# Performance work log

Measured on AMD Instinct MI355X. Metric: run time of the kernel, lower is better.

The kernel has to match this reference:

```python
import jax, jax.numpy as jnp
import numpy as np

NUM_HEADS = 12
WINDOW = 128
LOOK_B = 1
LOOK_F = 1


def look_around(x, pad_value):
    # x: (b, n_windows, window, ...) ; pad along window axis (axis=1), concat along axis=2
    pads = [(0, 0), (LOOK_B, LOOK_F)] + [(0, 0)] * (x.ndim - 2)
    p = jnp.pad(x, pads, constant_values=pad_value)
    n = x.shape[1]
    return jnp.concatenate([p[:, i:i + n] for i in range(LOOK_B + LOOK_F + 1)], axis=2)


def split_heads(x):
    # (L, B, D) -> (B*H, L, hd), batch-major over heads (index = b*H + h)
    L, B, D = x.shape
    return jnp.transpose(x.reshape(L, B * NUM_HEADS, D // NUM_HEADS), (1, 0, 2))


def merge_heads(x):
    # (B*H, L, hd) -> (L, B, D)
    BH, L, hd = x.shape
    return jnp.transpose(x, (1, 0, 2)).reshape(L, BH // NUM_HEADS, hd * NUM_HEADS)


def setup_inputs() -> dict:
    key = jax.random.key(0)
    ks = jax.random.split(key, 12)
    S, B, D = 4096, 8, 768
    inp = {
        'hidden_states': jax.random.normal(ks[0], (S, B, D), dtype=jnp.float32),
        'key_padding_mask': jax.random.bernoulli(ks[1], 0.2, (B, S)),
    }
    scale = 0.02
    for i, name in enumerate(['Wq', 'Wk', 'Wv', 'Wgq']):
        inp[name] = jax.random.normal(ks[2 + i], (D, D), dtype=jnp.float32) * scale
    for i, name in enumerate(['bq', 'bk', 'bv', 'bgq']):
        inp[name] = jax.random.normal(ks[6 + i], (D,), dtype=jnp.float32) * scale
    return inp


def reference(hidden_states, key_padding_mask, Wq, bq, Wk, bk, Wv, bv, Wgq, bgq):
    S, B, D = hidden_states.shape
    H, W = NUM_HEADS, WINDOW
    hd = D // H
    n = S // W
    BH = B * H
    neg = -jnp.finfo(hidden_states.dtype).max
    inv_sqrt = hd ** (-0.5)

    q = split_heads(hidden_states @ Wq + bq)  # (BH, S, hd)
    k = split_heads(hidden_states @ Wk + bk)
    v = split_heads(hidden_states @ Wv + bv)

    # --- local windowed attention ---
    bq_ = q.reshape(BH, n, W, hd)
    bk_ = look_around(k.reshape(BH, n, W, hd), 0.0)   # (BH, n, 3W, hd)
    bv_ = look_around(v.reshape(BH, n, W, hd), 0.0)
    dots = jnp.einsum('bnie,bnje->bnij', bq_, bk_) * inv_sqrt  # (BH, n, W, 3W)

    im = key_padding_mask.reshape(B, n, W)
    km = look_around(im, True)                        # (B, n, 3W), pads masked
    mask = im[:, :, :, None] | km[:, :, None, :]      # (B, n, W, 3W)
    mask = jnp.broadcast_to(mask[:, None], (B, H, n, W, 3 * W)).reshape(BH, n, W, 3 * W)
    dots = jnp.where(mask, neg, dots)
    attn = jax.nn.softmax(dots, axis=-1)
    out = jnp.einsum('bnij,bnje->bnie', attn, bv_).reshape(BH, S, hd)
    out = merge_heads(out)                            # (S, B, D)

    # --- global-token attention (token 0 attends to everything) ---
    gq = split_heads(hidden_states[0:1] @ Wgq + bgq)  # (BH, 1, hd)
    gdots = jnp.einsum('bie,bje->bij', gq, k) * inv_sqrt  # (BH, 1, S)
    gmask = jnp.broadcast_to(key_padding_mask[:, None], (B, H, S)).reshape(BH, S)
    gdots = jnp.where(gmask[:, None, :], neg, gdots)
    gattn = jax.nn.softmax(gdots, axis=-1)
    gout = merge_heads(jnp.einsum('bij,bje->bie', gattn, v))  # (1, B, D)

    return out.at[0].set(gout[0])
```

## Files before the change

kernel.cpp:

```cpp
#include <hip/hip_runtime.h>
#include <float.h>

#define S_  4096
#define B_  8
#define D_  768
#define H_  12
#define HD_ 64
#define W_  128
#define BH_ 96
#define SB_ 32768

typedef unsigned short u16;
typedef __attribute__((ext_vector_type(8))) short bf16x8;
typedef __attribute__((ext_vector_type(4))) float f32x4;

#define MFMA16(a,b,c) __builtin_amdgcn_mfma_f32_16x16x32_bf16(a,b,c,0,0,0)

__device__ __forceinline__ u16 f2bf(float x){
  unsigned int u = __float_as_uint(x);
  return (u16)((u + 0x7FFFu + ((u >> 16) & 1u)) >> 16);
}
__device__ __forceinline__ float bf2f(unsigned int lo16){ return __uint_as_float(lo16 << 16); }
__device__ __forceinline__ float bflo(unsigned int u){ return __uint_as_float(u << 16); }
__device__ __forceinline__ float bfhi(unsigned int u){ return __uint_as_float(u & 0xFFFF0000u); }
__device__ __forceinline__ unsigned int pk2(float a, float b){
  return (unsigned int)f2bf(a) | ((unsigned int)f2bf(b) << 16);
}

__device__ __forceinline__ void gload_lds16(const void* g, void* l){
  __builtin_amdgcn_global_load_lds(
      (const __attribute__((address_space(1))) void*)g,
      (__attribute__((address_space(3))) void*)l, 16, 0, 0);
}

__device__ __forceinline__ bool mask_at(const void* mp, int flag, int idx){
  return flag ? (((const unsigned char*)mp)[idx] != 0)
              : (((const unsigned int*)mp)[idx] != 0u);
}

__global__ __launch_bounds__(256) void prep_kernel(
    const float* __restrict__ hid, const float* __restrict__ W0,
    const float* __restrict__ W1, const float* __restrict__ W2,
    const unsigned int* __restrict__ maskw,
    u16* __restrict__ hb, u16* __restrict__ wT, int* __restrict__ flag){
  __shared__ float tile[64][65];
  const int bid = blockIdx.x, t = threadIdx.x;
  if (bid < 2048){
    int idx = bid * 256 + t;
    for (int base = idx * 8; base < 25165824; base += 2048 * 256 * 8){
      float4 a = *(const float4*)&hid[base];
      float4 b = *(const float4*)&hid[base + 4];
      uint4 o;
      o.x = pk2(a.x, a.y); o.y = pk2(a.z, a.w);
      o.z = pk2(b.x, b.y); o.w = pk2(b.z, b.w);
      *(uint4*)&hb[base] = o;
    }
  } else if (bid < 2480){
    const int wb = bid - 2048;
    const int mat = wb / 144, r2 = wb % 144;
    const int kt0 = (r2 / 12) * 64, nt0 = (r2 % 12) * 64;
    const float* Wsel = mat == 0 ? W0 : (mat == 1 ? W1 : W2);
    { const int row = t >> 2, c16 = (t & 3) * 16;
#pragma unroll
      for (int j = 0; j < 4; ++j){
        float4 v = *(const float4*)&Wsel[(size_t)(kt0 + row) * 768 + nt0 + c16 + j * 4];
        tile[row][c16 + j*4 + 0] = v.x; tile[row][c16 + j*4 + 1] = v.y;
        tile[row][c16 + j*4 + 2] = v.z; tile[row][c16 + j*4 + 3] = v.w;
      } }
    __syncthreads();
    { const int nl = t >> 2, k16 = (t & 3) * 16;
      unsigned int o[8];
#pragma unroll
      for (int j = 0; j < 8; ++j)
        o[j] = pk2(tile[k16 + 2*j][nl], tile[k16 + 2*j + 1][nl]);
      u16* dst = wT + (size_t)mat * 589824 + (size_t)(nt0 + nl) * 768 + kt0 + k16;
      *(uint4*)dst       = make_uint4(o[0], o[1], o[2], o[3]);
      *(uint4*)(dst + 8) = make_uint4(o[4], o[5], o[6], o[7]); }
  } else {
    unsigned int* red = (unsigned int*)&tile[0][0];
    unsigned int acc = 0u;
    for (int i = t; i < 8192; i += 256) acc |= maskw[i];
    red[t] = acc;
    __syncthreads();
    for (int s = 128; s > 0; s >>= 1){
      if (t < s) red[t] |= red[t + s];
      __syncthreads();
    }
    if (t == 0){
      unsigned int o = red[0];
      *flag = (o > 1u && (o & 0xFEFEFEFEu) == 0u) ? 1 : 0;
    }
  }
}

__global__ __launch_bounds__(256) void proj_mfma_kernel(
    const u16* __restrict__ hb, const u16* __restrict__ wT,
    const float* __restrict__ bq, const float* __restrict__ bk, const float* __restrict__ bv,
    u16* __restrict__ qb, u16* __restrict__ kb, u16* __restrict__ vb,
    u16* __restrict__ vtb){
  __shared__ union ShMem {
    struct { u16 A0[8192]; u16 B0[8192]; u16 A1[8192]; u16 B1[8192]; } ab;
    u16 C[128 * 130];
  } sh;
  const int t = threadIdx.x;
  const int id = blockIdx.x;
  const int xcd = id & 7, loc = id >> 3;
  const int nt = loc % 18;
  const int mt = xcd * 32 + loc / 18;
  const int p  = nt / 6;
  const int c0 = (nt % 6) * 128;
  const int r0 = mt * 128;
  const float* bias = p == 0 ? bq : (p == 1 ? bk : bv);
  u16* dst = p == 0 ? qb : (p == 1 ? kb : vb);
  const u16* wTp = wT + (size_t)p * 589824;

  const int lane = t & 63, w = t >> 6;
  const int l15 = lane & 15, lg = lane >> 4;
  const int wr = w >> 1, wc = w & 1;
  const int lrc = lane >> 3, slot = lane & 7;

  f32x4 acc[4][4] = {};

#define PSTAGE(AS, BS, kof) do{ \
    _Pragma("unroll") \
    for (int c = 0; c < 4; ++c){ \
      int chunk = w * 4 + c; \
      int ldsrow = chunk * 8 + lrc; \
      int slotg = slot ^ (ldsrow & 7); \
      gload_lds16(&hb [(size_t)(r0 + ldsrow) * 768 + (kof) + slotg * 8], &AS[chunk * 512]); \
      gload_lds16(&wTp[(size_t)(c0 + ldsrow) * 768 + (kof) + slotg * 8], &BS[chunk * 512]); \
    } \
  }while(0)

#define PITER(AS, BS, kof, VNSTR, DOSTAGE) do{ \
    asm volatile("s_waitcnt vmcnt(" VNSTR ")" ::: "memory"); \
    __builtin_amdgcn_sched_barrier(0); \
    __builtin_amdgcn_s_barrier(); \
    bf16x8 af[4][2], bf[4][2]; \
    _Pragma("unroll") \
    for (int mf = 0; mf < 4; ++mf) \
      _Pragma("unroll") \
      for (int ks = 0; ks < 2; ++ks) \
        af[mf][ks] = *(const bf16x8*)&AS[(wr*64 + mf*16 + l15) * 64 + (((ks*4 + lg) ^ (l15 & 7)) * 8)]; \
    _Pragma("unroll") \
    for (int nf = 0; nf < 4; ++nf) \
      _Pragma("unroll") \
      for (int ks = 0; ks < 2; ++ks) \
        bf[nf][ks] = *(const bf16x8*)&BS[(wc*64 + nf*16 + l15) * 64 + (((ks*4 + lg) ^ (l15 & 7)) * 8)]; \
    asm volatile("s_waitcnt lgkmcnt(0)" ::: "memory"); \
    __builtin_amdgcn_sched_barrier(0); \
    __builtin_amdgcn_s_barrier(); \
    if (DOSTAGE) PSTAGE(AS, BS, (kof) + 128); \
    _Pragma("unroll") \
    for (int ks = 0; ks < 2; ++ks) \
      _Pragma("unroll") \
      for (int mf = 0; mf < 4; ++mf) \
        _Pragma("unroll") \
        for (int nf = 0; nf < 4; ++nf) \
          acc[mf][nf] = MFMA16(af[mf][ks], bf[nf][ks], acc[mf][nf]); \
  }while(0)

  PSTAGE(sh.ab.A0, sh.ab.B0, 0);
  PSTAGE(sh.ab.A1, sh.ab.B1, 64);
  for (int i2 = 0; i2 < 5; ++i2){
    const int kc = i2 * 128;
    PITER(sh.ab.A0, sh.ab.B0, kc,      "8", 1);
    PITER(sh.ab.A1, sh.ab.B1, kc + 64, "8", 1);
  }
  PITER(sh.ab.A0, sh.ab.B0, 640, "8", 0);
  PITER(sh.ab.A1, sh.ab.B1, 704, "0", 0);
#undef PSTAGE
#undef PITER

#pragma unroll
  for (int nf = 0; nf < 4; ++nf){
    int c = c0 + wc*64 + nf*16 + l15;
    float bsv = bias[c];
#pragma unroll
    for (int mf = 0; mf < 4; ++mf)
#pragma unroll
      for (int r = 0; r < 4; ++r)
        sh.C[(wr*64 + mf*16 + lg*4 + r) * 130 + wc*64 + nf*16 + l15] = f2bf(acc[mf][nf][r] + bsv);
  }
  __syncthreads();
  { const int b = t >> 5, hh2 = (t >> 4) & 1, sl = t & 15;
    const int srow0 = r0 >> 3;
    const int hh = (c0 >> 6) + hh2;
    u16* dp = dst + ((size_t)(b * 12 + hh) * 4096 + srow0 + sl) * 64;
    const u16* sp = &sh.C[(sl * 8 + b) * 130 + hh2 * 64];
#pragma unroll
    for (int j = 0; j < 8; ++j)
      *(uint4*)(dp + j*8) = *(const uint4*)(sp + j*8);
  }
  if (p == 2){
    const int ri0 = t * 4;
#pragma unroll
    for (int j = 0; j < 4; ++j){
      const int ri = ri0 + j;
      const int b = ri >> 7, hh2 = (ri >> 6) & 1, dd = ri & 63;
      unsigned int o[8];
#pragma unroll
      for (int q = 0; q < 8; ++q){
        unsigned int lo = sh.C[((2*q    )*8 + b) * 130 + hh2*64 + dd];
        unsigned int hi = sh.C[((2*q + 1)*8 + b) * 130 + hh2*64 + dd];
        o[q] = lo | (hi << 16);
      }
      u16* dp2 = vtb + ((size_t)((b*12 + (c0 >> 6) + hh2) * 64) + dd) * 4096 + (r0 >> 3);
      *(uint4*)dp2       = make_uint4(o[0], o[1], o[2], o[3]);
      *(uint4*)(dp2 + 8) = make_uint4(o[4], o[5], o[6], o[7]);
    }
  }
}

__global__ __launch_bounds__(256) void local_mfma_kernel(
    const u16* __restrict__ qb, const u16* __restrict__ kb, const u16* __restrict__ vtb,
    const void* __restrict__ maskp, const int* __restrict__ flagp,
    float* __restrict__ out){
  __shared__ u16 KsA[64 * 64], KsB[64 * 64];
  __shared__ u16 VsA[64 * 64], VsB[64 * 64];
  __shared__ u16 Ps[4][32][72];
  __shared__ float kpen[384];
  __shared__ float qpen_s[128];
  const int t = threadIdx.x;
  const int id = blockIdx.x;
  const int swz = (id & 7) * 384 + (id >> 3);
  const int n_i = swz & 31, bh = swz >> 5;
  const int b_i = bh / 12, h = bh % 12;
  const int flag = *flagp;
  const int w = t >> 6, lane = t & 63, l15 = lane & 15, lg = lane >> 4;
  const int lrc = lane >> 3, slot = lane & 7;
  const int jbase0 = n_i * 128 - 128;
  const int jt_lo = (n_i == 0) ? 2 : 0;
  const int jt_hi = (n_i == 31) ? 4 : 6;

#define STAGE_TILE(KS, VS, jtv) do{ \
    int jb_ = jbase0 + (jtv) * 64; \
    _Pragma("unroll") \
    for (int c = 0; c < 2; ++c){ \
      int chunk = w * 2 + c; \
      int ldsrow = chunk * 8 + lrc; \
      int slotg = slot ^ (ldsrow & 7); \
      gload_lds16(&kb [((size_t)bh * 4096 + jb_ + ldsrow) * 64 + slotg * 8], &KS[chunk * 512]); \
      gload_lds16(&vtb[((size_t)bh * 64 + ldsrow) * 4096 + jb_ + slotg * 8], &VS[chunk * 512]); \
    } \
  }while(0)

#define COMPUTE_TILE(KS, VS, jtv) do{ \
    f32x4 dt[2][4] = {}; \
    __builtin_amdgcn_s_setprio(1); \
    _Pragma("unroll") \
    for (int ks2 = 0; ks2 < 2; ++ks2) \
      _Pragma("unroll") \
      for (int nf = 0; nf < 4; ++nf){ \
        bf16x8 bk_ = *(const bf16x8*)&KS[(nf*16 + l15) * 64 + (((ks2*4 + lg) ^ (l15 & 7)) * 8)]; \
        dt[0][nf] = MFMA16(bk_, aq[0][ks2], dt[0][nf]);    \
        dt[1][nf] = MFMA16(bk_, aq[1][ks2], dt[1][nf]); \
      } \
    __builtin_amdgcn_s_setprio(0); \
     \
    _Pragma("unroll") \
    for (int nf = 0; nf < 4; ++nf){ \
      float4 kpv = *(const float4*)&kpen[(jtv)*64 + nf*16 + lg*4]; \
      _Pragma("unroll") \
      for (int mf = 0; mf < 2; ++mf){ \
        dt[mf][nf][0] = (qp2[mf] + kpv.x == 0.f) ? dt[mf][nf][0] * 0.125f : -FLT_MAX; \
        dt[mf][nf][1] = (qp2[mf] + kpv.y == 0.f) ? dt[mf][nf][1] * 0.125f : -FLT_MAX; \
        dt[mf][nf][2] = (qp2[mf] + kpv.z == 0.f) ? dt[mf][nf][2] * 0.125f : -FLT_MAX; \
        dt[mf][nf][3] = (qp2[mf] + kpv.w == 0.f) ? dt[mf][nf][3] * 0.125f : -FLT_MAX; \
      } \
    } \
    _Pragma("unroll") \
    for (int mf = 0; mf < 2; ++mf){ \
      float tm = dt[mf][0][0]; \
      _Pragma("unroll") \
      for (int nf = 0; nf < 4; ++nf) \
        _Pragma("unroll") \
        for (int r = 0; r < 4; ++r) tm = fmaxf(tm, dt[mf][nf][r]); \
      tm = fmaxf(tm, __shfl_xor(tm, 16)); \
      tm = fmaxf(tm, __shfl_xor(tm, 32)); \
      float mold = mrow[mf]; \
      const bool up = (tm > mold + 8.f);         \
      float mnew = up ? tm : mold; \
      mrow[mf] = mnew; \
      float ps = 0.f; \
      _Pragma("unroll") \
      for (int nf = 0; nf < 4; ++nf) \
        _Pragma("unroll") \
        for (int r = 0; r < 4; ++r){ \
          float pv = __expf(dt[mf][nf][r] - mnew);    \
          ps += pv; \
          Ps[w][mf*16 + l15][nf*16 + lg*4 + r] = f2bf(pv); \
        } \
      float scl_own = up ? __expf(mold - mnew) : 1.0f; \
      ps += __shfl_xor(ps, 16); \
      ps += __shfl_xor(ps, 32); \
      lrow[mf] = lrow[mf] * scl_own + ps; \
      if (__any(up)){                           \
        _Pragma("unroll") \
        for (int r = 0; r < 4; ++r){ \
          float sr = __shfl(scl_own, lg*4 + r);   \
          _Pragma("unroll") \
          for (int nf = 0; nf < 4; ++nf) O[mf][nf][r] *= sr; \
        } \
      } \
    } \
    __builtin_amdgcn_s_setprio(1); \
    _Pragma("unroll") \
    for (int ks2 = 0; ks2 < 2; ++ks2){ \
      bf16x8 ap0 = *(const bf16x8*)&Ps[w][l15]     [ks2*32 + lg*8]; \
      bf16x8 ap1 = *(const bf16x8*)&Ps[w][16 + l15][ks2*32 + lg*8]; \
      _Pragma("unroll") \
      for (int nf = 0; nf < 4; ++nf){ \
        bf16x8 bv_ = *(const bf16x8*)&VS[(nf*16 + l15) * 64 + (((ks2*4 + lg) ^ (l15 & 7)) * 8)]; \
        O[0][nf] = MFMA16(ap0, bv_, O[0][nf]); \
        O[1][nf] = MFMA16(ap1, bv_, O[1][nf]); \
      } \
    } \
    __builtin_amdgcn_s_setprio(0); \
  }while(0)

  if (t < 128) qpen_s[t] = mask_at(maskp, flag, b_i * 4096 + n_i * 128 + t) ? 1.f : 0.f;
  for (int j = t; j < 384; j += 256){
    int jp = jbase0 + j;
    kpen[j] = (jp < 0 || jp >= 4096 || mask_at(maskp, flag, b_i * 4096 + jp)) ? 1.f : 0.f;
  }

  bf16x8 aq[2][2];
#pragma unroll
  for (int mf = 0; mf < 2; ++mf)
#pragma unroll
    for (int ks = 0; ks < 2; ++ks)
      aq[mf][ks] = *(const bf16x8*)&qb[((size_t)bh * 4096 + n_i*128 + w*32 + mf*16 + l15) * 64 + ks*32 + lg*8];

  STAGE_TILE(KsA, VsA, jt_lo);
  __syncthreads();

  float qp2[2];
#pragma unroll
  for (int mf = 0; mf < 2; ++mf)
    qp2[mf] = qpen_s[w*32 + mf*16 + l15];

  f32x4 O[2][4] = {};
  float mrow[2] = { -FLT_MAX, -FLT_MAX };
  float lrow[2] = { 0.f, 0.f };

  for (int base = jt_lo; base < jt_hi; base += 2){
    STAGE_TILE(KsB, VsB, base + 1);
    COMPUTE_TILE(KsA, VsA, base);
    __syncthreads();
    if (base + 2 < jt_hi) STAGE_TILE(KsA, VsA, base + 2);
    COMPUTE_TILE(KsB, VsB, base + 1);
    __syncthreads();
  }
#undef STAGE_TILE
#undef COMPUTE_TILE

  const float noor = (n_i == 0 || n_i == 31) ? 128.f : 0.f;
#pragma unroll
  for (int mf = 0; mf < 2; ++mf){
    float lf = lrow[mf] + ((mrow[mf] <= -FLT_MAX) ? noor : 0.f);
    float inv_own = 1.f / lf;
#pragma unroll
    for (int r = 0; r < 4; ++r){
      float inv = __shfl(inv_own, lg*4 + r);
      int srow = n_i*128 + w*32 + mf*16 + lg*4 + r;
      float* op = &out[(size_t)srow * (8 * 768) + b_i * 768 + h * 64];
#pragma unroll
      for (int nf = 0; nf < 4; ++nf)
        op[nf*16 + l15] = O[mf][nf][r] * inv;
    }
  }
}

__global__ __launch_bounds__(256) void gpart_kernel(
    const float* __restrict__ hid, const float* __restrict__ Wgq, const float* __restrict__ bgq,
    const u16* __restrict__ kb, const u16* __restrict__ vb,
    const void* __restrict__ maskp, const int* __restrict__ flagp,
    float* __restrict__ gp_out){
  __shared__ float hs[768];
  __shared__ float gqs[64];
  __shared__ float sc[512];
  __shared__ float red[256];
  const int t = threadIdx.x, bh = blockIdx.x, chunk = blockIdx.y;
  const int b_i = bh / 12, h = bh % 12;
  const int flag = *flagp;

  for (int c = t; c < 768; c += 256) hs[c] = hid[(size_t)b_i * 768 + c];
  __syncthreads();
  { const int dd = t & 63, part = t >> 6;
    float acc = 0.f;
    for (int c = part * 192; c < part * 192 + 192; ++c)
      acc += hs[c] * Wgq[(size_t)c * 768 + h * 64 + dd];
    red[t] = acc; }
  __syncthreads();
  if (t < 64)
    gqs[t] = (red[t] + red[t+64] + red[t+128] + red[t+192] + bgq[h*64 + t]) * 0.125f;
  __syncthreads();

#pragma unroll
  for (int i = 0; i < 2; ++i){
    int sl = i * 256 + t;
    int s = chunk * 512 + sl;
    const uint4* kr = (const uint4*)&kb[((size_t)bh * 4096 + s) * 64];
    float dot = 0.f;
#pragma unroll
    for (int u = 0; u < 8; ++u){
      uint4 x = kr[u];
      dot += gqs[u*8+0]*bflo(x.x) + gqs[u*8+1]*bfhi(x.x);
      dot += gqs[u*8+2]*bflo(x.y) + gqs[u*8+3]*bfhi(x.y);
      dot += gqs[u*8+4]*bflo(x.z) + gqs[u*8+5]*bfhi(x.z);
      dot += gqs[u*8+6]*bflo(x.w) + gqs[u*8+7]*bfhi(x.w);
    }
    sc[sl] = mask_at(maskp, flag, b_i * 4096 + s) ? -FLT_MAX : dot;
  }
  __syncthreads();
  float m = fmaxf(sc[t], sc[t + 256]);
  red[t] = m; __syncthreads();
  for (int st = 128; st > 0; st >>= 1){ if (t < st) red[t] = fmaxf(red[t], red[t + st]); __syncthreads(); }
  const float mc = red[0];
  __syncthreads();
  float ls = 0.f;
#pragma unroll
  for (int i = 0; i < 2; ++i){
    int sl = i * 256 + t;
    float p = __expf(sc[sl] - mc);
    sc[sl] = p; ls += p;
  }
  red[t] = ls; __syncthreads();
  for (int st = 128; st > 0; st >>= 1){ if (t < st) red[t] += red[t + st]; __syncthreads(); }
  const float lc = red[0];
  __syncthreads();
  const int dd = t & 63, part = t >> 6;
  float o = 0.f;
  for (int i2 = 0; i2 < 128; ++i2){
    int sl = part * 128 + i2;
    o += sc[sl] * bf2f(vb[((size_t)bh * 4096 + chunk * 512 + sl) * 64 + dd]);
  }
  red[t] = o; __syncthreads();
  float* gp = gp_out + ((size_t)bh * 8 + chunk) * 66;
  if (t == 0){ gp[0] = mc; gp[1] = lc; }
  if (t < 64) gp[2 + t] = red[t] + red[t+64] + red[t+128] + red[t+192];
}

__global__ __launch_bounds__(64) void greduce_kernel(const float* __restrict__ gp_in,
                                                     float* __restrict__ out){
  const int t = threadIdx.x, bh = blockIdx.x, b_i = bh / 12, h = bh % 12;
  const float* gp = gp_in + (size_t)bh * 8 * 66;
  float mg = -FLT_MAX;
#pragma unroll
  for (int c = 0; c < 8; ++c) mg = fmaxf(mg, gp[c * 66]);
  float lg = 0.f, o = 0.f;
#pragma unroll
  for (int c = 0; c < 8; ++c){
    float wv = __expf(gp[c * 66] - mg);
    lg += gp[c * 66 + 1] * wv;
    o  += gp[c * 66 + 2 + t] * wv;
  }
  out[(size_t)b_i * 768 + h * 64 + t] = o / lg;
}

extern "C" void kernel_launch(void* const* d_in, const int* in_sizes, int n_in,
                              void* d_out, int out_size, void* d_ws, size_t ws_size,
                              hipStream_t stream) {
  const float* hid   = (const float*)d_in[0];
  const void*  maskp = d_in[1];
  const float* Wq  = (const float*)d_in[2];
  const float* Wk  = (const float*)d_in[3];
  const float* Wv  = (const float*)d_in[4];
  const float* Wgq = (const float*)d_in[5];
  const float* bq  = (const float*)d_in[6];
  const float* bk  = (const float*)d_in[7];
  const float* bv  = (const float*)d_in[8];
  const float* bgq = (const float*)d_in[9];
  float* out = (float*)d_out;

  char* wsb = (char*)d_ws;
  int* flag   = (int*)wsb;
  u16* hb     = (u16*)(wsb + 256);
  u16* wT     = (u16*)(wsb + 50331904);
  u16* qb     = (u16*)(wsb + 53870848);
  u16* kb     = (u16*)(wsb + 104202496);
  u16* vb     = (u16*)(wsb + 154534144);
  u16* vtb    = (u16*)(wsb + 204865792);
  float* gpart = (float*)(wsb + 255222016);

  prep_kernel<<<2481, 256, 0, stream>>>(hid, Wq, Wk, Wv,
                                        (const unsigned int*)maskp, hb, wT, flag);
  proj_mfma_kernel<<<4608, 256, 0, stream>>>(hb, wT, bq, bk, bv, qb, kb, vb, vtb);
  local_mfma_kernel<<<3072, 256, 0, stream>>>(qb, kb, vtb, maskp, flag, out);
  gpart_kernel<<<dim3(96, 8), 256, 0, stream>>>(hid, Wgq, bgq, kb, vb, maskp, flag, gpart);
  greduce_kernel<<<96, 64, 0, stream>>>(gpart, out);
}
```

Baseline: 367.9 us.

## Widen QKV projection tile to 128x256 and group rows by batch

The projection GEMM tile grows from 128x128 to 128x256 output columns, covering four heads, so each A tile is reused across twice as many columns. The grid shrinks to half as many blocks. The M tile now takes 128 sequence positions of a single batch, using strided row loads, so the writeback to the head-major q/k/v and transposed v buffers becomes contiguous per head. The cost is double the accumulator registers and LDS for B, which lowers occupancy.

Result: no change. 365.3 us (-0.7%).

```diff
diff --git a/kernel.cpp b/kernel.cpp
--- a/kernel.cpp
+++ b/kernel.cpp
@@ -99,35 +99,43 @@
     u16* __restrict__ qb, u16* __restrict__ kb, u16* __restrict__ vb,
     u16* __restrict__ vtb){
   __shared__ union ShMem {
-    struct { u16 A0[8192]; u16 B0[8192]; u16 A1[8192]; u16 B1[8192]; } ab;
-    u16 C[128 * 130];
+    struct { u16 A0[8192]; u16 B0[16384]; u16 A1[8192]; u16 B1[16384]; } ab;
+    u16 C[128 * 264];
   } sh;
   const int t = threadIdx.x;
   const int id = blockIdx.x;
   const int xcd = id & 7, loc = id >> 3;
-  const int nt = loc % 18;
-  const int mt = xcd * 32 + loc / 18;
-  const int p  = nt / 6;
-  const int c0 = (nt % 6) * 128;
-  const int r0 = mt * 128;
+  const int nt = loc % 9;
+  const int mt = xcd * 32 + loc / 9;
+  const int p  = nt / 3;
+  const int c0 = (nt % 3) * 256;
+  const int b0 = mt >> 5;
+  const int s0 = (mt & 31) * 128;
   const float* bias = p == 0 ? bq : (p == 1 ? bk : bv);
   u16* dst = p == 0 ? qb : (p == 1 ? kb : vb);
   const u16* wTp = wT + (size_t)p * 589824;
+  const int hhbase = c0 >> 6;
 
   const int lane = t & 63, w = t >> 6;
   const int l15 = lane & 15, lg = lane >> 4;
   const int wr = w >> 1, wc = w & 1;
   const int lrc = lane >> 3, slot = lane & 7;
 
-  f32x4 acc[4][4] = {};
+  f32x4 acc[4][8] = {};
 
 #define PSTAGE(AS, BS, kof) do{ \
     _Pragma("unroll") \
-    for (int c = 0; c < 4; ++c){ \
+    for (int c = 0; c < 4; ++c){             \
       int chunk = w * 4 + c; \
-      int ldsrow = chunk * 8 + lrc; \
+      int ldsrow = chunk * 8 + lrc;          \
       int slotg = slot ^ (ldsrow & 7); \
-      gload_lds16(&hb [(size_t)(r0 + ldsrow) * 768 + (kof) + slotg * 8], &AS[chunk * 512]); \
+      gload_lds16(&hb[((size_t)(s0 + ldsrow) * 8 + b0) * 768 + (kof) + slotg * 8], &AS[chunk * 512]); \
+    } \
+    _Pragma("unroll") \
+    for (int c = 0; c < 8; ++c){             \
+      int chunk = w * 8 + c; \
+      int ldsrow = chunk * 8 + lrc;          \
+      int slotg = slot ^ (ldsrow & 7); \
       gload_lds16(&wTp[(size_t)(c0 + ldsrow) * 768 + (kof) + slotg * 8], &BS[chunk * 512]); \
     } \
   }while(0)
@@ -136,17 +144,17 @@
     asm volatile("s_waitcnt vmcnt(" VNSTR ")" ::: "memory"); \
     __builtin_amdgcn_sched_barrier(0); \
     __builtin_amdgcn_s_barrier(); \
-    bf16x8 af[4][2], bf[4][2]; \
+    bf16x8 af[4][2], bf[8][2]; \
     _Pragma("unroll") \
     for (int mf = 0; mf < 4; ++mf) \
       _Pragma("unroll") \
       for (int ks = 0; ks < 2; ++ks) \
         af[mf][ks] = *(const bf16x8*)&AS[(wr*64 + mf*16 + l15) * 64 + (((ks*4 + lg) ^ (l15 & 7)) * 8)]; \
     _Pragma("unroll") \
-    for (int nf = 0; nf < 4; ++nf) \
+    for (int nf = 0; nf < 8; ++nf) \
       _Pragma("unroll") \
       for (int ks = 0; ks < 2; ++ks) \
-        bf[nf][ks] = *(const bf16x8*)&BS[(wc*64 + nf*16 + l15) * 64 + (((ks*4 + lg) ^ (l15 & 7)) * 8)]; \
+        bf[nf][ks] = *(const bf16x8*)&BS[(wc*128 + nf*16 + l15) * 64 + (((ks*4 + lg) ^ (l15 & 7)) * 8)]; \
     asm volatile("s_waitcnt lgkmcnt(0)" ::: "memory"); \
     __builtin_amdgcn_sched_barrier(0); \
     __builtin_amdgcn_s_barrier(); \
@@ -156,7 +164,7 @@
       _Pragma("unroll") \
       for (int mf = 0; mf < 4; ++mf) \
         _Pragma("unroll") \
-        for (int nf = 0; nf < 4; ++nf) \
+        for (int nf = 0; nf < 8; ++nf) \
           acc[mf][nf] = MFMA16(af[mf][ks], bf[nf][ks], acc[mf][nf]); \
   }while(0)
 
@@ -164,50 +172,53 @@
   PSTAGE(sh.ab.A1, sh.ab.B1, 64);
   for (int i2 = 0; i2 < 5; ++i2){
     const int kc = i2 * 128;
-    PITER(sh.ab.A0, sh.ab.B0, kc,      "8", 1);
-    PITER(sh.ab.A1, sh.ab.B1, kc + 64, "8", 1);
-  }
-  PITER(sh.ab.A0, sh.ab.B0, 640, "8", 0);
+    PITER(sh.ab.A0, sh.ab.B0, kc,      "12", 1);
+    PITER(sh.ab.A1, sh.ab.B1, kc + 64, "12", 1);
+  }
+  PITER(sh.ab.A0, sh.ab.B0, 640, "12", 0);
   PITER(sh.ab.A1, sh.ab.B1, 704, "0", 0);
 #undef PSTAGE
 #undef PITER
 
 #pragma unroll
-  for (int nf = 0; nf < 4; ++nf){
-    int c = c0 + wc*64 + nf*16 + l15;
+  for (int nf = 0; nf < 8; ++nf){
+    int c = c0 + wc*128 + nf*16 + l15;
     float bsv = bias[c];
 #pragma unroll
     for (int mf = 0; mf < 4; ++mf)
 #pragma unroll
       for (int r = 0; r < 4; ++r)
-        sh.C[(wr*64 + mf*16 + lg*4 + r) * 130 + wc*64 + nf*16 + l15] = f2bf(acc[mf][nf][r] + bsv);
-  }
-  __syncthreads();
-  { const int b = t >> 5, hh2 = (t >> 4) & 1, sl = t & 15;
-    const int srow0 = r0 >> 3;
-    const int hh = (c0 >> 6) + hh2;
-    u16* dp = dst + ((size_t)(b * 12 + hh) * 4096 + srow0 + sl) * 64;
-    const u16* sp = &sh.C[(sl * 8 + b) * 130 + hh2 * 64];
+        sh.C[(wr*64 + mf*16 + lg*4 + r) * 264 + wc*128 + nf*16 + l15] = f2bf(acc[mf][nf][r] + bsv);
+  }
+  __syncthreads();
+#pragma unroll
+  for (int rep = 0; rep < 2; ++rep){
+    const int task = rep * 256 + t;
+    const int srow = task & 127, hh4 = task >> 7;
+    u16* dp = dst + ((size_t)(b0 * 12 + hhbase + hh4) * 4096 + s0 + srow) * 64;
+    const u16* sp = &sh.C[srow * 264 + hh4 * 64];
 #pragma unroll
     for (int j = 0; j < 8; ++j)
       *(uint4*)(dp + j*8) = *(const uint4*)(sp + j*8);
   }
   if (p == 2){
-    const int ri0 = t * 4;
-#pragma unroll
-    for (int j = 0; j < 4; ++j){
-      const int ri = ri0 + j;
-      const int b = ri >> 7, hh2 = (ri >> 6) & 1, dd = ri & 63;
-      unsigned int o[8];
+#pragma unroll
+    for (int rep = 0; rep < 2; ++rep){
+      const int task = rep * 256 + t;
+      const int dd = task & 63, sHalf = (task >> 6) & 1, hh4 = task >> 7;
+      u16* dp2 = vtb + ((size_t)((b0*12 + hhbase + hh4) * 64) + dd) * 4096 + s0 + sHalf * 64;
 #pragma unroll
       for (int q = 0; q < 8; ++q){
-        unsigned int lo = sh.C[((2*q    )*8 + b) * 130 + hh2*64 + dd];
-        unsigned int hi = sh.C[((2*q + 1)*8 + b) * 130 + hh2*64 + dd];
-        o[q] = lo | (hi << 16);
+        unsigned int ow[4];
+#pragma unroll
+        for (int j = 0; j < 4; ++j){
+          const int srow = sHalf*64 + q*8 + 2*j;
+          unsigned int lo = sh.C[srow * 264 + hh4*64 + dd];
+          unsigned int hi = sh.C[(srow + 1) * 264 + hh4*64 + dd];
+          ow[j] = lo | (hi << 16);
+        }
+        *(uint4*)(dp2 + q*8) = make_uint4(ow[0], ow[1], ow[2], ow[3]);
       }
-      u16* dp2 = vtb + ((size_t)((b*12 + (c0 >> 6) + hh2) * 64) + dd) * 4096 + (r0 >> 3);
-      *(uint4*)dp2       = make_uint4(o[0], o[1], o[2], o[3]);
-      *(uint4*)(dp2 + 8) = make_uint4(o[4], o[5], o[6], o[7]);
     }
   }
 }
@@ -298,7 +309,7 @@
       if (__any(up)){                           \
         _Pragma("unroll") \
         for (int r = 0; r < 4; ++r){ \
-          float sr = __shfl(scl_own, lg*4 + r);   \
+          float sr = __shfl(scl_own, lg*4 + r); \
           _Pragma("unroll") \
           for (int nf = 0; nf < 4; ++nf) O[mf][nf][r] *= sr; \
         } \
@@ -486,7 +497,7 @@
 
   prep_kernel<<<2481, 256, 0, stream>>>(hid, Wq, Wk, Wv,
                                         (const unsigned int*)maskp, hb, wT, flag);
-  proj_mfma_kernel<<<4608, 256, 0, stream>>>(hb, wT, bq, bk, bv, qb, kb, vb, vtb);
+  proj_mfma_kernel<<<2304, 256, 0, stream>>>(hb, wT, bq, bk, bv, qb, kb, vb, vtb);
   local_mfma_kernel<<<3072, 256, 0, stream>>>(qb, kb, vtb, maskp, flag, out);
   gpart_kernel<<<dim3(96, 8), 256, 0, stream>>>(hid, Wgq, bgq, kb, vb, maskp, flag, gpart);
   greduce_kernel<<<96, 64, 0, stream>>>(gpart, out);
```

## Tile projection rows per batch and pack softmax probabilities into wide LDS stores

Applied to the files above, without the earlier changes.

The projection kernel now assigns each 128-row M tile to a single batch and a contiguous sequence range, reading hidden_states with a strided (s*8+b) address. Each thread can then write Q/K/V rows contiguously, and the V-transpose store emits 16-byte chunks along the sequence axis instead of gathering across batches. In the local attention kernel, four exp results are packed into one 8-byte LDS store rather than four scalar bf16 stores. The aim is to cut scattered global writes and LDS store count, at the cost of less contiguous A-operand loads from hidden_states.

New measurement: 350.3 us (median of 2 runs). 1.05x faster.

```diff
diff --git a/kernel.cpp b/kernel.cpp
--- a/kernel.cpp
+++ b/kernel.cpp
@@ -109,10 +109,12 @@
   const int mt = xcd * 32 + loc / 18;
   const int p  = nt / 6;
   const int c0 = (nt % 6) * 128;
-  const int r0 = mt * 128;
+  const int b0 = mt >> 5;
+  const int s0 = (mt & 31) * 128;
   const float* bias = p == 0 ? bq : (p == 1 ? bk : bv);
   u16* dst = p == 0 ? qb : (p == 1 ? kb : vb);
   const u16* wTp = wT + (size_t)p * 589824;
+  const int hhbase = c0 >> 6;
 
   const int lane = t & 63, w = t >> 6;
   const int l15 = lane & 15, lg = lane >> 4;
@@ -125,9 +127,9 @@
     _Pragma("unroll") \
     for (int c = 0; c < 4; ++c){ \
       int chunk = w * 4 + c; \
-      int ldsrow = chunk * 8 + lrc; \
+      int ldsrow = chunk * 8 + lrc;          \
       int slotg = slot ^ (ldsrow & 7); \
-      gload_lds16(&hb [(size_t)(r0 + ldsrow) * 768 + (kof) + slotg * 8], &AS[chunk * 512]); \
+      gload_lds16(&hb[((size_t)(s0 + ldsrow) * 8 + b0) * 768 + (kof) + slotg * 8], &AS[chunk * 512]); \
       gload_lds16(&wTp[(size_t)(c0 + ldsrow) * 768 + (kof) + slotg * 8], &BS[chunk * 512]); \
     } \
   }while(0)
@@ -183,31 +185,28 @@
         sh.C[(wr*64 + mf*16 + lg*4 + r) * 130 + wc*64 + nf*16 + l15] = f2bf(acc[mf][nf][r] + bsv);
   }
   __syncthreads();
-  { const int b = t >> 5, hh2 = (t >> 4) & 1, sl = t & 15;
-    const int srow0 = r0 >> 3;
-    const int hh = (c0 >> 6) + hh2;
-    u16* dp = dst + ((size_t)(b * 12 + hh) * 4096 + srow0 + sl) * 64;
-    const u16* sp = &sh.C[(sl * 8 + b) * 130 + hh2 * 64];
+  { const int srow = t & 127, hh2 = t >> 7;
+    u16* dp = dst + ((size_t)(b0 * 12 + hhbase + hh2) * 4096 + s0 + srow) * 64;
+    const u16* sp = &sh.C[srow * 130 + hh2 * 64];
 #pragma unroll
     for (int j = 0; j < 8; ++j)
       *(uint4*)(dp + j*8) = *(const uint4*)(sp + j*8);
   }
   if (p == 2){
-    const int ri0 = t * 4;
-#pragma unroll
-    for (int j = 0; j < 4; ++j){
-      const int ri = ri0 + j;
-      const int b = ri >> 7, hh2 = (ri >> 6) & 1, dd = ri & 63;
-      unsigned int o[8];
-#pragma unroll
-      for (int q = 0; q < 8; ++q){
-        unsigned int lo = sh.C[((2*q    )*8 + b) * 130 + hh2*64 + dd];
-        unsigned int hi = sh.C[((2*q + 1)*8 + b) * 130 + hh2*64 + dd];
-        o[q] = lo | (hi << 16);
+    const int sHalf = t & 1, pair = t >> 1;
+    const int dd = pair & 63, hh2 = pair >> 6;
+    u16* dp2 = vtb + ((size_t)((b0*12 + hhbase + hh2) * 64) + dd) * 4096 + s0 + sHalf * 64;
+#pragma unroll
+    for (int q = 0; q < 8; ++q){
+      unsigned int ow[4];
+#pragma unroll
+      for (int j = 0; j < 4; ++j){
+        const int srow = sHalf*64 + q*8 + 2*j;
+        unsigned int lo = sh.C[srow * 130 + hh2*64 + dd];
+        unsigned int hi = sh.C[(srow + 1) * 130 + hh2*64 + dd];
+        ow[j] = lo | (hi << 16);
       }
-      u16* dp2 = vtb + ((size_t)((b*12 + (c0 >> 6) + hh2) * 64) + dd) * 4096 + (r0 >> 3);
-      *(uint4*)dp2       = make_uint4(o[0], o[1], o[2], o[3]);
-      *(uint4*)(dp2 + 8) = make_uint4(o[4], o[5], o[6], o[7]);
+      *(uint4*)(dp2 + q*8) = make_uint4(ow[0], ow[1], ow[2], ow[3]);
     }
   }
 }
@@ -284,13 +283,15 @@
       mrow[mf] = mnew; \
       float ps = 0.f; \
       _Pragma("unroll") \
-      for (int nf = 0; nf < 4; ++nf) \
-        _Pragma("unroll") \
-        for (int r = 0; r < 4; ++r){ \
-          float pv = __expf(dt[mf][nf][r] - mnew);    \
-          ps += pv; \
-          Ps[w][mf*16 + l15][nf*16 + lg*4 + r] = f2bf(pv); \
-        } \
+      for (int nf = 0; nf < 4; ++nf){ \
+        float pv0 = __expf(dt[mf][nf][0] - mnew); \
+        float pv1 = __expf(dt[mf][nf][1] - mnew); \
+        float pv2 = __expf(dt[mf][nf][2] - mnew); \
+        float pv3 = __expf(dt[mf][nf][3] - mnew); \
+        ps += pv0 + pv1 + pv2 + pv3; \
+        uint2 w2; w2.x = pk2(pv0, pv1); w2.y = pk2(pv2, pv3); \
+        *(uint2*)&Ps[w][mf*16 + l15][nf*16 + lg*4] = w2;    \
+      } \
       float scl_own = up ? __expf(mold - mnew) : 1.0f; \
       ps += __shfl_xor(ps, 16); \
       ps += __shfl_xor(ps, 32); \
@@ -298,7 +299,7 @@
       if (__any(up)){                           \
         _Pragma("unroll") \
         for (int r = 0; r < 4; ++r){ \
-          float sr = __shfl(scl_own, lg*4 + r);   \
+          float sr = __shfl(scl_own, lg*4 + r); \
           _Pragma("unroll") \
           for (int nf = 0; nf < 4; ++nf) O[mf][nf][r] *= sr; \
         } \
```
